# Kernel optimization log

Hardware: AMD Instinct MI355X
Metric: run time of the kernel (lower is better)

Reference implementation:

```python
import jax, jax.numpy as jnp
import numpy as np

D_MODEL = 256
N_HEADS_SA = 8
CA_HEADS = 8
CA_DH = 64
CA_INNER = CA_HEADS * CA_DH  # 512
N_POINTS = 4
D_FFN = 1024
OFFSET_SCALE = 2.0
B, NQ = 4, 1024
T, H, W = 4, 64, 64
LV = T * H * W

PNAMES = ['sa_Wq','sa_bq','sa_Wk','sa_bk','sa_Wv','sa_bv','sa_Wo','sa_bo',
          'ln1_g','ln1_b','ln2_g','ln2_b','ln3_g','ln3_b',
          'ca_Wq','ca_bq','ca_Wk','ca_bk','ca_Wv','ca_bv','ca_Wref','ca_bref',
          'ca_Woff','ca_boff','ca_Wo','ca_bo',
          'ffn_W1','ffn_b1','ffn_W2','ffn_b2']


def _layer_norm(x, g, b, eps=1e-5):
    m = x.mean(-1, keepdims=True)
    v = ((x - m) ** 2).mean(-1, keepdims=True)
    return (x - m) * jax.lax.rsqrt(v + eps) * g + b


def _mha(q, k, v, Wq, bq, Wk, bk, Wv, bv, Wo, bo, n_heads):
    Bq, N, D = q.shape
    dh = D // n_heads
    scale = 1.0 / float(np.sqrt(dh))
    qh = (q @ Wq + bq).reshape(Bq, N, n_heads, dh)
    kh = (k @ Wk + bk).reshape(Bq, N, n_heads, dh)
    vh = (v @ Wv + bv).reshape(Bq, N, n_heads, dh)
    attn = jax.nn.softmax(jnp.einsum('bqhd,bkhd->bhqk', qh, kh) * scale, -1)
    out = jnp.einsum('bhqk,bkhd->bqhd', attn, vh).reshape(Bq, N, D)
    return out @ Wo + bo


def _trilinear_sample(vol, loc, sizes_f):
    # vol: [B, L, Hd, dh] flattened (T*H*W) volume per head
    # loc: [B, N, Hd, P, 3] normalized (t, h, w) coords in [0, 1]
    Bv, L, Hd, dh = vol.shape
    _, N, _, P, _ = loc.shape
    pos = jnp.clip(loc, 0.0, 1.0) * (sizes_f - 1.0)  # align_corners voxel coords
    p0 = jnp.floor(pos)
    frac = pos - p0
    p0i = p0.astype(jnp.int32)
    sizes_i = sizes_f.astype(jnp.int32)
    Hn, Wn = sizes_i[1], sizes_i[2]
    vol_t = vol.transpose(0, 2, 1, 3)  # [B, Hd, L, dh]
    out = jnp.zeros((Bv, Hd, N * P, dh), vol.dtype)
    for dt in (0, 1):
        for dy in (0, 1):
            for dx in (0, 1):
                c = jnp.minimum(p0i + jnp.array([dt, dy, dx], jnp.int32), sizes_i - 1)
                wt = (frac[..., 0] if dt else 1.0 - frac[..., 0]) \
                   * (frac[..., 1] if dy else 1.0 - frac[..., 1]) \
                   * (frac[..., 2] if dx else 1.0 - frac[..., 2])  # [B,N,Hd,P]
                idx = c[..., 0] * (Hn * Wn) + c[..., 1] * Wn + c[..., 2]
                idx_t = idx.transpose(0, 2, 1, 3).reshape(Bv, Hd, N * P, 1)
                g = jnp.take_along_axis(vol_t, idx_t, axis=2)  # [B,Hd,N*P,dh]
                w_t = wt.transpose(0, 2, 1, 3).reshape(Bv, Hd, N * P, 1)
                out = out + g * w_t
    return out.reshape(Bv, Hd, N, P, dh).transpose(0, 2, 1, 3, 4)  # [B,N,Hd,P,dh]


def _deform_cross_attn(query, key, value, flow_key, flow_value, spatial_shapes, p):
    Bq, N, _ = query.shape
    L = key.shape[1]
    sizes_f = spatial_shapes[0].astype(jnp.float32)  # single level (T, H, W)
    qh = (query @ p['ca_Wq'] + p['ca_bq']).reshape(Bq, N, CA_HEADS, CA_DH)
    ref = jax.nn.sigmoid(query @ p['ca_Wref'] + p['ca_bref'])  # [B,N,3]
    off = (query @ p['ca_Woff'] + p['ca_boff']).reshape(Bq, N, CA_HEADS, N_POINTS, 3)
    loc = ref[:, :, None, None, :] + off * (OFFSET_SCALE / sizes_f)
    k_vol = (key @ p['ca_Wk'] + p['ca_bk']).reshape(Bq, L, CA_HEADS, CA_DH)
    v_vol = (value @ p['ca_Wv'] + p['ca_bv']).reshape(Bq, L, CA_HEADS, CA_DH)
    fk_vol = (flow_key @ p['ca_Wk'] + p['ca_bk']).reshape(Bq, L, CA_HEADS, CA_DH)
    fv_vol = (flow_value @ p['ca_Wv'] + p['ca_bv']).reshape(Bq, L, CA_HEADS, CA_DH)
    k_s = _trilinear_sample(k_vol, loc, sizes_f)
    v_s = _trilinear_sample(v_vol, loc, sizes_f)
    fk_s = _trilinear_sample(fk_vol, loc, sizes_f)
    fv_s = _trilinear_sample(fv_vol, loc, sizes_f)
    scale = 1.0 / float(np.sqrt(CA_DH))
    logits = jnp.concatenate([
        jnp.einsum('bnhd,bnhpd->bnhp', qh, k_s),
        jnp.einsum('bnhd,bnhpd->bnhp', qh, fk_s)], -1) * scale
    attn = jax.nn.softmax(logits, -1)  # joint softmax over image+flow sampled points
    vals = jnp.concatenate([v_s, fv_s], 3)  # [B,N,Hd,2P,dh]
    out = jnp.einsum('bnhp,bnhpd->bnhd', attn, vals).reshape(Bq, N, CA_INNER)
    return out @ p['ca_Wo'] + p['ca_bo']


def _forward(query, query_pos, img, flow, pos_emb, spatial_shapes, p):
    q = query + query_pos
    sa = _mha(q, q, query, p['sa_Wq'], p['sa_bq'], p['sa_Wk'], p['sa_bk'],
              p['sa_Wv'], p['sa_bv'], p['sa_Wo'], p['sa_bo'], N_HEADS_SA)
    x = _layer_norm(query + sa, p['ln1_g'], p['ln1_b'])
    key = pos_emb + img
    flow_key = pos_emb + flow
    ca = _deform_cross_attn(x, key, img, flow_key, flow, spatial_shapes, p)
    x = _layer_norm(x + ca, p['ln2_g'], p['ln2_b'])
    ffn = jax.nn.relu(x @ p['ffn_W1'] + p['ffn_b1']) @ p['ffn_W2'] + p['ffn_b2']
    return _layer_norm(x + ffn, p['ln3_g'], p['ln3_b'])


def setup_inputs() -> dict:
    key = jax.random.key(0)
    ks = iter(jax.random.split(key, 64))
    def rn(shape, s=1.0):
        return jax.random.normal(next(ks), shape, jnp.float32) * s
    inp = {
        'query': rn((B, NQ, D_MODEL)),
        'query_pos': rn((B, NQ, D_MODEL)),
        'img_embed_flatten': rn((B, LV, D_MODEL)),
        'flow_embed_flatten': rn((B, LV, D_MODEL)),
        'indicator_temporal_lvl_pos_embed_flatten': rn((B, LV, D_MODEL)),
        'spatial_shapes': jnp.array([[T, H, W]], jnp.int32),
    }
    for nm in ['sa_Wq', 'sa_Wk', 'sa_Wv', 'sa_Wo']:
        inp[nm] = rn((D_MODEL, D_MODEL), 0.02)
    for nm in ['sa_bq', 'sa_bk', 'sa_bv', 'sa_bo', 'ln1_b', 'ln2_b', 'ln3_b']:
        inp[nm] = jnp.zeros((D_MODEL,), jnp.float32)
    for nm in ['ln1_g', 'ln2_g', 'ln3_g']:
        inp[nm] = jnp.ones((D_MODEL,), jnp.float32)
    inp['ca_Wq'] = rn((D_MODEL, CA_INNER), 0.02); inp['ca_bq'] = jnp.zeros((CA_INNER,), jnp.float32)
    inp['ca_Wk'] = rn((D_MODEL, CA_INNER), 0.02); inp['ca_bk'] = jnp.zeros((CA_INNER,), jnp.float32)
    inp['ca_Wv'] = rn((D_MODEL, CA_INNER), 0.02); inp['ca_bv'] = jnp.zeros((CA_INNER,), jnp.float32)
    inp['ca_Wref'] = rn((D_MODEL, 3), 0.02); inp['ca_bref'] = jnp.zeros((3,), jnp.float32)
    inp['ca_Woff'] = rn((D_MODEL, CA_HEADS * N_POINTS * 3), 0.02)
    inp['ca_boff'] = jnp.zeros((CA_HEADS * N_POINTS * 3,), jnp.float32)
    inp['ca_Wo'] = rn((CA_INNER, D_MODEL), 0.02); inp['ca_bo'] = jnp.zeros((D_MODEL,), jnp.float32)
    inp['ffn_W1'] = rn((D_MODEL, D_FFN), 0.02); inp['ffn_b1'] = jnp.zeros((D_FFN,), jnp.float32)
    inp['ffn_W2'] = rn((D_FFN, D_MODEL), 0.02); inp['ffn_b2'] = jnp.zeros((D_MODEL,), jnp.float32)
    return inp


def reference(query, query_pos, img_embed_flatten, flow_embed_flatten,
              indicator_temporal_lvl_pos_embed_flatten, spatial_shapes,
              sa_Wq, sa_bq, sa_Wk, sa_bk, sa_Wv, sa_bv, sa_Wo, sa_bo,
              ln1_g, ln1_b, ln2_g, ln2_b, ln3_g, ln3_b,
              ca_Wq, ca_bq, ca_Wk, ca_bk, ca_Wv, ca_bv, ca_Wref, ca_bref,
              ca_Woff, ca_boff, ca_Wo, ca_bo,
              ffn_W1, ffn_b1, ffn_W2, ffn_b2):
    p = dict(zip(PNAMES, (sa_Wq, sa_bq, sa_Wk, sa_bk, sa_Wv, sa_bv, sa_Wo, sa_bo,
                          ln1_g, ln1_b, ln2_g, ln2_b, ln3_g, ln3_b,
                          ca_Wq, ca_bq, ca_Wk, ca_bk, ca_Wv, ca_bv, ca_Wref, ca_bref,
                          ca_Woff, ca_boff, ca_Wo, ca_bo,
                          ffn_W1, ffn_b1, ffn_W2, ffn_b2)))
    return _forward(query, query_pos, img_embed_flatten, flow_embed_flatten,
                    indicator_temporal_lvl_pos_embed_flatten, spatial_shapes, p)
```

## Files before the change

kernel.cpp:

```cpp
#include <hip/hip_runtime.h>
#include <hip/hip_bf16.h>

#define BQ 4
#define NQT 1024
#define DM 256
#define HSA 8
#define DHSA 32
#define CAH 8
#define CADH 64
#define CAI 512
#define NPT 4
#define DFFN 1024
#define TT 4
#define HH 64
#define WW 64
#define LVOL 16384

using bf16 = __hip_bfloat16;
typedef __attribute__((ext_vector_type(4))) float fx4;
typedef __attribute__((ext_vector_type(8))) short s8v;
typedef __attribute__((ext_vector_type(4))) short s4v;

__device__ __forceinline__ float b2f(bf16 v) { return __bfloat162float(v); }
__device__ __forceinline__ bf16  f2b(float v) { return __float2bfloat16(v); }
__device__ __forceinline__ short f2bs(float v) {
  bf16 b = __float2bfloat16(v);
  return *reinterpret_cast<short*>(&b);
}

__device__ __forceinline__ float wave_sum64(float v) {
#pragma unroll
  for (int o = 32; o >= 1; o >>= 1) v += __shfl_xor(v, o, 64);
  return v;
}

__device__ __forceinline__ s8v pack8(float4 a, float4 b) {
  return (s8v){f2bs(a.x), f2bs(a.y), f2bs(a.z), f2bs(a.w),
               f2bs(b.x), f2bs(b.y), f2bs(b.z), f2bs(b.w)};
}

template <int KSH>
__global__ __launch_bounds__(256) void wtrans_k(const float* __restrict__ W,
                                               short* __restrict__ Wt, int N) {
  const int i = blockIdx.x * 256 + threadIdx.x;
  const int k = i & ((1 << KSH) - 1);
  const int n = i >> KSH;
  Wt[i] = f2bs(W[(size_t)k * N + n]);
}

template <int DUAL, int RELU, int OUTBF>
__global__ __launch_bounds__(256) void mgemm_k(
    const float* __restrict__ A, const float* __restrict__ A2,
    const short* __restrict__ Wt, const float* __restrict__ bias,
    void* __restrict__ Cout, int M, int N, int K) {
  __shared__ short As[2][128 * 40];
  __shared__ short Bs[2][128 * 40];
  const int tid = threadIdx.x;
  const int lane = tid & 63, w = tid >> 6;
  const int wr = w >> 1, wc = w & 1;
  const int lm = lane & 15, quad = lane >> 4;
  const int nwg = gridDim.x * gridDim.y;
  const int ib = blockIdx.y * gridDim.x + blockIdx.x;
  const int id = (ib & 7) * (nwg >> 3) + (ib >> 3);
  const int m0 = (id / gridDim.x) * 128;
  const int n0 = (id % gridDim.x) * 128;

  const int am = tid >> 3, ak = (tid & 7) * 4;

  float4 pa[4], pa2[4];
  s8v pb[2];
  auto loadT = [&](int k0) {
#pragma unroll
    for (int i = 0; i < 4; i++) {
      pa[i] = *(const float4*)&A[(size_t)(m0 + am + i * 32) * K + k0 + ak];
      if (DUAL)
        pa2[i] = *(const float4*)&A2[(size_t)(m0 + am + i * 32) * K + k0 + ak];
    }
#pragma unroll
    for (int i = 0; i < 2; i++) {
      int unit = tid + i * 256;
      pb[i] = *(const s8v*)&Wt[(size_t)(n0 + (unit >> 2)) * K + k0 +
                               (unit & 3) * 8];
    }
  };
  auto stageT = [&](int buf) {
#pragma unroll
    for (int i = 0; i < 4; i++) {
      float x0 = pa[i].x, x1 = pa[i].y, x2 = pa[i].z, x3 = pa[i].w;
      if (DUAL) { x0 += pa2[i].x; x1 += pa2[i].y; x2 += pa2[i].z; x3 += pa2[i].w; }
      s4v sv = {f2bs(x0), f2bs(x1), f2bs(x2), f2bs(x3)};
      *(s4v*)&As[buf][(am + i * 32) * 40 + ak] = sv;
    }
#pragma unroll
    for (int i = 0; i < 2; i++) {
      int unit = tid + i * 256;
      *(s8v*)&Bs[buf][(unit >> 2) * 40 + (unit & 3) * 8] = pb[i];
    }
  };

  fx4 acc[4][4] = {};
  loadT(0);
  stageT(0);
  __syncthreads();
  int cur = 0;
  for (int k0 = 0; k0 < K; k0 += 32) {
    const int more = (k0 + 32 < K);
    if (more) loadT(k0 + 32);
    s8v af[4], bfr[4];
#pragma unroll
    for (int f = 0; f < 4; f++) {
      af[f] = *(s8v*)&As[cur][(wr * 64 + f * 16 + lm) * 40 + quad * 8];
      bfr[f] = *(s8v*)&Bs[cur][(wc * 64 + f * 16 + lm) * 40 + quad * 8];
    }
#pragma unroll
    for (int fm = 0; fm < 4; fm++)
#pragma unroll
      for (int fn = 0; fn < 4; fn++)
        acc[fm][fn] = __builtin_amdgcn_mfma_f32_16x16x32_bf16(
            af[fm], bfr[fn], acc[fm][fn], 0, 0, 0);
    if (more) stageT(cur ^ 1);
    __syncthreads();
    cur ^= 1;
  }
#pragma unroll
  for (int fn = 0; fn < 4; fn++) {
    const int n = n0 + wc * 64 + fn * 16 + lm;
    const float bb = bias[n];
#pragma unroll
    for (int fm = 0; fm < 4; fm++) {
      const int mbase = m0 + wr * 64 + fm * 16 + quad * 4;
#pragma unroll
      for (int r = 0; r < 4; r++) {
        float v = acc[fm][fn][r] + bb;
        if (RELU) v = fmaxf(v, 0.0f);
        const size_t off = (size_t)(mbase + r) * N + n;
        if (OUTBF)
          ((bf16*)Cout)[off] = f2b(v);
        else
          ((float*)Cout)[off] = v;
      }
    }
  }
}

__global__ __launch_bounds__(256) void sa_flash_k(
    const float* __restrict__ qh, const float* __restrict__ kh,
    const float* __restrict__ vh, float* __restrict__ outp) {
  __shared__ short Ks[64 * 72];
  __shared__ short Vt[32 * 72];
  __shared__ short Ps[64 * 72];
  const int qt = blockIdx.x, h = blockIdx.y, b = blockIdx.z;
  const int tid = threadIdx.x;
  const int w = tid >> 6, lane = tid & 63;
  const int lm = lane & 15, quad = lane >> 4;
  const size_t rowbase = (size_t)(b * NQT) * DM + h * DHSA;

  s8v aq;
  {
    const int qrow = qt * 64 + w * 16 + lm;
    const float* qp = &qh[rowbase + (size_t)qrow * DM + quad * 8];
    const float4 q0 = *(const float4*)qp;
    const float4 q1 = *(const float4*)(qp + 4);
    const float sc = 0.17677669529663687f;
    aq = (s8v){f2bs(q0.x * sc), f2bs(q0.y * sc), f2bs(q0.z * sc), f2bs(q0.w * sc),
               f2bs(q1.x * sc), f2bs(q1.y * sc), f2bs(q1.z * sc), f2bs(q1.w * sc)};
  }

  fx4 o0 = {}, o1 = {};
  float mrun[4] = {-1e30f, -1e30f, -1e30f, -1e30f};
  float lrun[4] = {0.f, 0.f, 0.f, 0.f};
  const int jr = tid >> 2;
  const int d0 = (tid & 3) * 8;

  for (int jt = 0; jt < 16; jt++) {
    __syncthreads();
    {
      const size_t rb = rowbase + (size_t)(jt * 64 + jr) * DM + d0;
      const float4 k0 = *(const float4*)&kh[rb];
      const float4 k1 = *(const float4*)&kh[rb + 4];
      *(s8v*)&Ks[jr * 72 + d0] = pack8(k0, k1);
      const float4 v0 = *(const float4*)&vh[rb];
      const float4 v1 = *(const float4*)&vh[rb + 4];
      Vt[(d0 + 0) * 72 + jr] = f2bs(v0.x);
      Vt[(d0 + 1) * 72 + jr] = f2bs(v0.y);
      Vt[(d0 + 2) * 72 + jr] = f2bs(v0.z);
      Vt[(d0 + 3) * 72 + jr] = f2bs(v0.w);
      Vt[(d0 + 4) * 72 + jr] = f2bs(v1.x);
      Vt[(d0 + 5) * 72 + jr] = f2bs(v1.y);
      Vt[(d0 + 6) * 72 + jr] = f2bs(v1.z);
      Vt[(d0 + 7) * 72 + jr] = f2bs(v1.w);
    }
    __syncthreads();
    fx4 s[4];
    const fx4 zero = {};
#pragma unroll
    for (int nf = 0; nf < 4; nf++) {
      s8v kb = *(const s8v*)&Ks[(nf * 16 + lm) * 72 + quad * 8];
      s[nf] = __builtin_amdgcn_mfma_f32_16x16x32_bf16(aq, kb, zero, 0, 0, 0);
    }
#pragma unroll
    for (int r = 0; r < 4; r++) {
      float mx = fmaxf(fmaxf(s[0][r], s[1][r]), fmaxf(s[2][r], s[3][r]));
#pragma unroll
      for (int off = 8; off >= 1; off >>= 1)
        mx = fmaxf(mx, __shfl_xor(mx, off, 64));
      const float mnew = fmaxf(mrun[r], mx);
      const float corr = expf(mrun[r] - mnew);
      mrun[r] = mnew;
      float p0 = expf(s[0][r] - mnew);
      float p1 = expf(s[1][r] - mnew);
      float p2 = expf(s[2][r] - mnew);
      float p3 = expf(s[3][r] - mnew);
      float rs = p0 + p1 + p2 + p3;
#pragma unroll
      for (int off = 8; off >= 1; off >>= 1) rs += __shfl_xor(rs, off, 64);
      lrun[r] = lrun[r] * corr + rs;
      o0[r] *= corr;
      o1[r] *= corr;
      s[0][r] = p0; s[1][r] = p1; s[2][r] = p2; s[3][r] = p3;
    }
#pragma unroll
    for (int nf = 0; nf < 4; nf++)
#pragma unroll
      for (int r = 0; r < 4; r++)
        Ps[(w * 16 + quad * 4 + r) * 72 + nf * 16 + lm] = f2bs(s[nf][r]);
#pragma unroll
    for (int ks = 0; ks < 2; ks++) {
      s8v pf = *(const s8v*)&Ps[(w * 16 + lm) * 72 + ks * 32 + quad * 8];
      s8v vb0 = *(const s8v*)&Vt[lm * 72 + ks * 32 + quad * 8];
      s8v vb1 = *(const s8v*)&Vt[(16 + lm) * 72 + ks * 32 + quad * 8];
      o0 = __builtin_amdgcn_mfma_f32_16x16x32_bf16(pf, vb0, o0, 0, 0, 0);
      o1 = __builtin_amdgcn_mfma_f32_16x16x32_bf16(pf, vb1, o1, 0, 0, 0);
    }
  }
#pragma unroll
  for (int r = 0; r < 4; r++) {
    const float inv = 1.0f / lrun[r];
    const size_t base =
        rowbase + (size_t)(qt * 64 + w * 16 + quad * 4 + r) * DM;
    outp[base + lm] = o0[r] * inv;
    outp[base + 16 + lm] = o1[r] * inv;
  }
}

__global__ __launch_bounds__(128) void refoff_k(
    const float* __restrict__ x1, const float* __restrict__ Wref,
    const float* __restrict__ bref, const float* __restrict__ Woff,
    const float* __restrict__ boff, float* __restrict__ refb,
    float* __restrict__ offb) {
  __shared__ float xs[256];
  const int row = blockIdx.x;
  const int tid = threadIdx.x;
  xs[tid] = x1[(size_t)row * DM + tid];
  xs[tid + 128] = x1[(size_t)row * DM + tid + 128];
  __syncthreads();
  if (tid < 3) {
    float s = bref[tid];
    for (int d = 0; d < 256; d++) s = fmaf(xs[d], Wref[d * 3 + tid], s);
    refb[(size_t)row * 3 + tid] = 1.0f / (1.0f + expf(-s));
  } else if (tid < 99) {
    int o = tid - 3;
    float s = boff[o];
    for (int d = 0; d < 256; d++) s = fmaf(xs[d], Woff[d * 96 + o], s);
    offb[(size_t)row * 96 + o] = s;
  }
}

__device__ __forceinline__ void calc_corners(
    const float* __restrict__ refb, const float* __restrict__ offb, int bn,
    int h, int (&idxs)[NPT][8], float (&wts)[NPT][8]) {
  const float rt = refb[bn * 3 + 0], ry = refb[bn * 3 + 1], rx = refb[bn * 3 + 2];
  const float* ofp = &offb[(size_t)bn * 96 + h * 12];
#pragma unroll
  for (int p = 0; p < NPT; p++) {
    float lt = rt + ofp[p * 3 + 0] * 0.5f;
    float ly = ry + ofp[p * 3 + 1] * 0.03125f;
    float lx = rx + ofp[p * 3 + 2] * 0.03125f;
    float pt = fminf(fmaxf(lt, 0.f), 1.f) * (TT - 1);
    float py = fminf(fmaxf(ly, 0.f), 1.f) * (HH - 1);
    float px = fminf(fmaxf(lx, 0.f), 1.f) * (WW - 1);
    float f0t = floorf(pt), f0y = floorf(py), f0x = floorf(px);
    float frt = pt - f0t, fry = py - f0y, frx = px - f0x;
    int t0 = (int)f0t, y0 = (int)f0y, x0 = (int)f0x;
    int t1 = min(t0 + 1, TT - 1), y1 = min(y0 + 1, HH - 1), x1 = min(x0 + 1, WW - 1);
    float wt0 = 1.f - frt, wy0 = 1.f - fry, wx0 = 1.f - frx;
#pragma unroll
    for (int c = 0; c < 8; c++) {
      int dt = c >> 2, dy = (c >> 1) & 1, dx = c & 1;
      int ct = dt ? t1 : t0, cy = dy ? y1 : y0, cx = dx ? x1 : x0;
      idxs[p][c] = ct * (HH * WW) + cy * WW + cx;
      wts[p][c] = (dt ? frt : wt0) * (dy ? fry : wy0) * (dx ? frx : wx0);
    }
  }
}

__global__ __launch_bounds__(256) void ca_logits_k(
    const float* __restrict__ qh, const float* __restrict__ refb,
    const float* __restrict__ offb, const bf16* __restrict__ vol,
    float* __restrict__ logits, int slot) {
  const int wid = (blockIdx.x * blockDim.x + threadIdx.x) >> 6;
  const int lane = threadIdx.x & 63;
  const int h = wid & 7;
  const int bn = wid >> 3;
  const int b = bn >> 10;
  const float q = qh[(size_t)bn * CAI + h * CADH + lane];
  int idxs[NPT][8];
  float wts[NPT][8];
  calc_corners(refb, offb, bn, h, idxs, wts);
  const size_t volbase = (size_t)b * LVOL * CAI + h * CADH + lane;
  float* lp = logits + ((size_t)bn * CAH + h) * 8 + slot;
#pragma unroll
  for (int p = 0; p < NPT; p++) {
    float ks = 0.f;
#pragma unroll
    for (int c = 0; c < 8; c++)
      ks = fmaf(wts[p][c], b2f(vol[volbase + (size_t)idxs[p][c] * CAI]), ks);
    float li = wave_sum64(q * ks) * 0.125f;
    if (lane == p) lp[p] = li;
  }
}

__global__ __launch_bounds__(256) void ca_softmax_k(float* __restrict__ logits) {
  const int i = blockIdx.x * blockDim.x + threadIdx.x;
  float* p = logits + (size_t)i * 8;
  float v[8], m = -1e30f;
#pragma unroll
  for (int j = 0; j < 8; j++) { v[j] = p[j]; m = fmaxf(m, v[j]); }
  float s = 0.f;
#pragma unroll
  for (int j = 0; j < 8; j++) { v[j] = expf(v[j] - m); s += v[j]; }
  const float inv = 1.0f / s;
#pragma unroll
  for (int j = 0; j < 8; j++) p[j] = v[j] * inv;
}

template <int FIRST>
__global__ __launch_bounds__(256) void ca_acc_k(
    const float* __restrict__ refb, const float* __restrict__ offb,
    const bf16* __restrict__ vol, const float* __restrict__ attn,
    float* __restrict__ acc, int slot) {
  const int wid = (blockIdx.x * blockDim.x + threadIdx.x) >> 6;
  const int lane = threadIdx.x & 63;
  const int h = wid & 7;
  const int bn = wid >> 3;
  const int b = bn >> 10;
  int idxs[NPT][8];
  float wts[NPT][8];
  calc_corners(refb, offb, bn, h, idxs, wts);
  const size_t volbase = (size_t)b * LVOL * CAI + h * CADH + lane;
  const float* ap = attn + ((size_t)bn * CAH + h) * 8 + slot;
  const size_t off = (size_t)bn * CAI + h * CADH + lane;
  float a = FIRST ? 0.f : acc[off];
#pragma unroll
  for (int p = 0; p < NPT; p++) {
    float vs = 0.f;
#pragma unroll
    for (int c = 0; c < 8; c++)
      vs = fmaf(wts[p][c], b2f(vol[volbase + (size_t)idxs[p][c] * CAI]), vs);
    a = fmaf(ap[p], vs, a);
  }
  acc[off] = a;
}

__global__ __launch_bounds__(256) void ln_k(
    const float* __restrict__ resv, const float* __restrict__ x,
    const float* __restrict__ g, const float* __restrict__ bb,
    float* __restrict__ of) {
  const int row = (blockIdx.x * blockDim.x + threadIdx.x) >> 6;
  const int lane = threadIdx.x & 63;
  const size_t base = (size_t)row * DM;
  float v[4];
#pragma unroll
  for (int i = 0; i < 4; i++) {
    int d = lane + i * 64;
    v[i] = resv[base + d] + x[base + d];
  }
  float s = wave_sum64(v[0] + v[1] + v[2] + v[3]);
  const float mean = s * (1.0f / 256.0f);
  float vs = 0.f;
#pragma unroll
  for (int i = 0; i < 4; i++) { float d0 = v[i] - mean; vs = fmaf(d0, d0, vs); }
  vs = wave_sum64(vs);
  const float rstd = rsqrtf(vs * (1.0f / 256.0f) + 1e-5f);
#pragma unroll
  for (int i = 0; i < 4; i++) {
    int d = lane + i * 64;
    of[base + d] = (v[i] - mean) * rstd * g[d] + bb[d];
  }
}

extern "C" void kernel_launch(void* const* d_in, const int* in_sizes, int n_in,
                              void* d_out, int out_size, void* d_ws,
                              size_t ws_size, hipStream_t stream) {
  const float* query = (const float*)d_in[0];
  const float* qpos = (const float*)d_in[1];
  const float* img = (const float*)d_in[2];
  const float* flow = (const float*)d_in[3];
  const float* pos = (const float*)d_in[4];
  const float* sa_Wq = (const float*)d_in[6];
  const float* sa_Wk = (const float*)d_in[7];
  const float* sa_Wv = (const float*)d_in[8];
  const float* sa_Wo = (const float*)d_in[9];
  const float* sa_bq = (const float*)d_in[10];
  const float* sa_bk = (const float*)d_in[11];
  const float* sa_bv = (const float*)d_in[12];
  const float* sa_bo = (const float*)d_in[13];
  const float* ln1_b = (const float*)d_in[14];
  const float* ln2_b = (const float*)d_in[15];
  const float* ln3_b = (const float*)d_in[16];
  const float* ln1_g = (const float*)d_in[17];
  const float* ln2_g = (const float*)d_in[18];
  const float* ln3_g = (const float*)d_in[19];
  const float* ca_Wq = (const float*)d_in[20];
  const float* ca_bq = (const float*)d_in[21];
  const float* ca_Wk = (const float*)d_in[22];
  const float* ca_bk = (const float*)d_in[23];
  const float* ca_Wv = (const float*)d_in[24];
  const float* ca_bv = (const float*)d_in[25];
  const float* ca_Wref = (const float*)d_in[26];
  const float* ca_bref = (const float*)d_in[27];
  const float* ca_Woff = (const float*)d_in[28];
  const float* ca_boff = (const float*)d_in[29];
  const float* ca_Wo = (const float*)d_in[30];
  const float* ca_bo = (const float*)d_in[31];
  const float* ffn_W1 = (const float*)d_in[32];
  const float* ffn_b1 = (const float*)d_in[33];
  const float* ffn_W2 = (const float*)d_in[34];
  const float* ffn_b2 = (const float*)d_in[35];

  const int MQ = BQ * NQT;
  const int MV = BQ * LVOL;
  const size_t MB = 1024 * 1024;

  char* r0 = (char*)d_ws;
  char* w = r0 + 64 * MB;
  auto alloc = [&](size_t n) {
    char* p = w;
    w += (n + 255) & ~(size_t)255;
    return p;
  };
  float* x1_f = (float*)alloc((size_t)MQ * DM * 4);
  float* ca_qh = (float*)alloc((size_t)MQ * CAI * 4);
  float* refb = (float*)alloc((size_t)MQ * 3 * 4);
  float* offb = (float*)alloc((size_t)MQ * 96 * 4);
  float* logits = (float*)alloc((size_t)MQ * CAH * 8 * 4);
  float* ca_acc = (float*)alloc((size_t)MQ * CAI * 4);
  short* WtsaQ = (short*)alloc((size_t)DM * DM * 2);
  short* WtsaK = (short*)alloc((size_t)DM * DM * 2);
  short* WtsaV = (short*)alloc((size_t)DM * DM * 2);
  short* WtsaO = (short*)alloc((size_t)DM * DM * 2);
  short* Wtcaq = (short*)alloc((size_t)CAI * DM * 2);
  short* Wtk = (short*)alloc((size_t)CAI * DM * 2);
  short* Wtv = (short*)alloc((size_t)CAI * DM * 2);
  short* Wtcao = (short*)alloc((size_t)DM * CAI * 2);
  short* Wtf1 = (short*)alloc((size_t)DFFN * DM * 2);
  short* Wtf2 = (short*)alloc((size_t)DM * DFFN * 2);
  if ((size_t)(w - (char*)d_ws) > ws_size) return;

  float* qh_sa = (float*)(r0 + 0 * MB);
  float* kh_sa = (float*)(r0 + 4 * MB);
  float* vh_sa = (float*)(r0 + 8 * MB);
  float* sa_att = (float*)(r0 + 12 * MB);
  float* sa_proj = (float*)(r0 + 16 * MB);
  bf16* vol = (bf16*)r0;
  float* ca_o = (float*)(r0 + 0 * MB);
  float* x2_f = (float*)(r0 + 4 * MB);
  float* ffn_h = (float*)(r0 + 8 * MB);
  float* ffn_o = (float*)(r0 + 24 * MB);

  dim3 blk(256);
  wtrans_k<8><<<dim3(DM * DM / 256), blk, 0, stream>>>(sa_Wq, WtsaQ, DM);
  wtrans_k<8><<<dim3(DM * DM / 256), blk, 0, stream>>>(sa_Wk, WtsaK, DM);
  wtrans_k<8><<<dim3(DM * DM / 256), blk, 0, stream>>>(sa_Wv, WtsaV, DM);
  wtrans_k<8><<<dim3(DM * DM / 256), blk, 0, stream>>>(sa_Wo, WtsaO, DM);
  wtrans_k<8><<<dim3(DM * CAI / 256), blk, 0, stream>>>(ca_Wq, Wtcaq, CAI);
  wtrans_k<8><<<dim3(DM * CAI / 256), blk, 0, stream>>>(ca_Wk, Wtk, CAI);
  wtrans_k<8><<<dim3(DM * CAI / 256), blk, 0, stream>>>(ca_Wv, Wtv, CAI);
  wtrans_k<8><<<dim3(DM * DFFN / 256), blk, 0, stream>>>(ffn_W1, Wtf1, DFFN);
  wtrans_k<9><<<dim3(CAI * DM / 256), blk, 0, stream>>>(ca_Wo, Wtcao, DM);
  wtrans_k<10><<<dim3(DFFN * DM / 256), blk, 0, stream>>>(ffn_W2, Wtf2, DM);
  mgemm_k<1, 0, 0><<<dim3(DM / 128, MQ / 128), blk, 0, stream>>>(query, qpos, WtsaQ, sa_bq, (void*)qh_sa, MQ, DM, DM);
  mgemm_k<1, 0, 0><<<dim3(DM / 128, MQ / 128), blk, 0, stream>>>(query, qpos, WtsaK, sa_bk, (void*)kh_sa, MQ, DM, DM);
  mgemm_k<0, 0, 0><<<dim3(DM / 128, MQ / 128), blk, 0, stream>>>(query, query, WtsaV, sa_bv, (void*)vh_sa, MQ, DM, DM);
  sa_flash_k<<<dim3(16, 8, 4), blk, 0, stream>>>(qh_sa, kh_sa, vh_sa, sa_att);
  mgemm_k<0, 0, 0><<<dim3(DM / 128, MQ / 128), blk, 0, stream>>>(sa_att, sa_att, WtsaO, sa_bo, (void*)sa_proj, MQ, DM, DM);
  ln_k<<<dim3(MQ / 4), blk, 0, stream>>>(query, sa_proj, ln1_g, ln1_b, x1_f);
  mgemm_k<0, 0, 0><<<dim3(CAI / 128, MQ / 128), blk, 0, stream>>>(x1_f, x1_f, Wtcaq, ca_bq, (void*)ca_qh, MQ, CAI, DM);
  refoff_k<<<dim3(MQ), dim3(128), 0, stream>>>(x1_f, ca_Wref, ca_bref, ca_Woff, ca_boff, refb, offb);
  mgemm_k<1, 0, 1><<<dim3(CAI / 128, MV / 128), blk, 0, stream>>>(pos, img, Wtk, ca_bk, (void*)vol, MV, CAI, DM);
  ca_logits_k<<<dim3(8192), blk, 0, stream>>>(ca_qh, refb, offb, vol, logits, 0);
  mgemm_k<1, 0, 1><<<dim3(CAI / 128, MV / 128), blk, 0, stream>>>(pos, flow, Wtk, ca_bk, (void*)vol, MV, CAI, DM);
  ca_logits_k<<<dim3(8192), blk, 0, stream>>>(ca_qh, refb, offb, vol, logits, 4);
  ca_softmax_k<<<dim3(128), blk, 0, stream>>>(logits);
  mgemm_k<0, 0, 1><<<dim3(CAI / 128, MV / 128), blk, 0, stream>>>(img, img, Wtv, ca_bv, (void*)vol, MV, CAI, DM);
  ca_acc_k<1><<<dim3(8192), blk, 0, stream>>>(refb, offb, vol, logits, ca_acc, 0);
  mgemm_k<0, 0, 1><<<dim3(CAI / 128, MV / 128), blk, 0, stream>>>(flow, flow, Wtv, ca_bv, (void*)vol, MV, CAI, DM);
  ca_acc_k<0><<<dim3(8192), blk, 0, stream>>>(refb, offb, vol, logits, ca_acc, 4);
  mgemm_k<0, 0, 0><<<dim3(DM / 128, MQ / 128), blk, 0, stream>>>(ca_acc, ca_acc, Wtcao, ca_bo, (void*)ca_o, MQ, DM, CAI);
  ln_k<<<dim3(MQ / 4), blk, 0, stream>>>(x1_f, ca_o, ln2_g, ln2_b, x2_f);
  mgemm_k<0, 1, 0><<<dim3(DFFN / 128, MQ / 128), blk, 0, stream>>>(x2_f, x2_f, Wtf1, ffn_b1, (void*)ffn_h, MQ, DFFN, DM);
  mgemm_k<0, 0, 0><<<dim3(DM / 128, MQ / 128), blk, 0, stream>>>(ffn_h, ffn_h, Wtf2, ffn_b2, (void*)ffn_o, MQ, DM, DFFN);
  ln_k<<<dim3(MQ / 4), blk, 0, stream>>>(x2_f, ffn_o, ln3_g, ln3_b, (float*)d_out);
}
```

Measured before the change: 744.6 us.

## Pre-convert volume inputs to bf16 and use direct-to-LDS loads in volume GEMMs

The four large K/V projection GEMMs over the flattened volume now run in two steps. A prep kernel first adds the positional embedding where needed and converts the fp32 input to a bf16 buffer. A new bf16 GEMM then streams that buffer and the transposed weights straight into LDS with global_load_lds, double buffered, and feeds MFMA. The aim is to take fp32 loading and conversion out of the GEMM main loop, where the A tile is re-read once per N-block, and to overlap global loads with compute without staging through registers. The cost is an extra read and write pass over each volume input, plus new unpadded LDS tiles that may cause bank conflicts.

```diff
diff --git a/kernel.cpp b/kernel.cpp
--- a/kernel.cpp
+++ b/kernel.cpp
@@ -39,6 +39,12 @@
                f2bs(b.x), f2bs(b.y), f2bs(b.z), f2bs(b.w)};
 }
 
+__device__ __forceinline__ void gl_lds16(const void* g, void* l) {
+  __builtin_amdgcn_global_load_lds(
+      (const __attribute__((address_space(1))) unsigned int*)g,
+      (__attribute__((address_space(3))) unsigned int*)l, 16, 0, 0);
+}
+
 template <int KSH>
 __global__ __launch_bounds__(256) void wtrans_k(const float* __restrict__ W,
                                                short* __restrict__ Wt, int N) {
@@ -46,6 +52,91 @@
   const int k = i & ((1 << KSH) - 1);
   const int n = i >> KSH;
   Wt[i] = f2bs(W[(size_t)k * N + n]);
+}
+
+template <int DUAL>
+__global__ __launch_bounds__(256) void prep_k(const float* __restrict__ A,
+                                              const float* __restrict__ B,
+                                              short* __restrict__ O, int n8) {
+  for (int i = blockIdx.x * 256 + threadIdx.x; i < n8; i += gridDim.x * 256) {
+    float4 a0 = *(const float4*)&A[(size_t)i * 8];
+    float4 a1 = *(const float4*)&A[(size_t)i * 8 + 4];
+    if (DUAL) {
+      const float4 b0 = *(const float4*)&B[(size_t)i * 8];
+      const float4 b1 = *(const float4*)&B[(size_t)i * 8 + 4];
+      a0.x += b0.x; a0.y += b0.y; a0.z += b0.z; a0.w += b0.w;
+      a1.x += b1.x; a1.y += b1.y; a1.z += b1.z; a1.w += b1.w;
+    }
+    *(s8v*)&O[(size_t)i * 8] = pack8(a0, a1);
+  }
+}
+
+__global__ __launch_bounds__(256) void bgemm_k(
+    const short* __restrict__ A, const short* __restrict__ Wt,
+    const float* __restrict__ bias, bf16* __restrict__ Cout,
+    int M, int N, int K) {
+  __shared__ short As[2][128 * 32];
+  __shared__ short Bs[2][128 * 32];
+  const int tid = threadIdx.x;
+  const int lane = tid & 63, w = tid >> 6;
+  const int wr = w >> 1, wc = w & 1;
+  const int lm = lane & 15, quad = lane >> 4;
+  const int nwg = gridDim.x * gridDim.y;
+  const int ib = blockIdx.y * gridDim.x + blockIdx.x;
+  const int id = (ib & 7) * (nwg >> 3) + (ib >> 3);
+  const int m0 = (id / gridDim.x) * 128;
+  const int n0 = (id % gridDim.x) * 128;
+
+  const int srow = lane >> 2;
+  const int scol = (lane & 3) * 8;
+  const size_t arow = (size_t)(m0 + w * 32 + srow);
+  const size_t brow = (size_t)(n0 + w * 32 + srow);
+
+  fx4 acc[4][4] = {};
+  const int nt = K / 32;
+  int cur = 0;
+  {
+    gl_lds16(&A[arow * K + scol], &As[0][(w * 32) * 32]);
+    gl_lds16(&A[(arow + 16) * K + scol], &As[0][(w * 32 + 16) * 32]);
+    gl_lds16(&Wt[brow * K + scol], &Bs[0][(w * 32) * 32]);
+    gl_lds16(&Wt[(brow + 16) * K + scol], &Bs[0][(w * 32 + 16) * 32]);
+  }
+  __syncthreads();
+  for (int t = 0; t < nt; t++) {
+    if (t + 1 < nt) {
+      const int k0 = (t + 1) * 32;
+      gl_lds16(&A[arow * K + k0 + scol], &As[cur ^ 1][(w * 32) * 32]);
+      gl_lds16(&A[(arow + 16) * K + k0 + scol], &As[cur ^ 1][(w * 32 + 16) * 32]);
+      gl_lds16(&Wt[brow * K + k0 + scol], &Bs[cur ^ 1][(w * 32) * 32]);
+      gl_lds16(&Wt[(brow + 16) * K + k0 + scol], &Bs[cur ^ 1][(w * 32 + 16) * 32]);
+    }
+    s8v af[4], bfr[4];
+#pragma unroll
+    for (int f = 0; f < 4; f++) {
+      af[f] = *(s8v*)&As[cur][(wr * 64 + f * 16 + lm) * 32 + quad * 8];
+      bfr[f] = *(s8v*)&Bs[cur][(wc * 64 + f * 16 + lm) * 32 + quad * 8];
+    }
+#pragma unroll
+    for (int fm = 0; fm < 4; fm++)
+#pragma unroll
+      for (int fn = 0; fn < 4; fn++)
+        acc[fm][fn] = __builtin_amdgcn_mfma_f32_16x16x32_bf16(
+            af[fm], bfr[fn], acc[fm][fn], 0, 0, 0);
+    __syncthreads();
+    cur ^= 1;
+  }
+#pragma unroll
+  for (int fn = 0; fn < 4; fn++) {
+    const int n = n0 + wc * 64 + fn * 16 + lm;
+    const float bb = bias[n];
+#pragma unroll
+    for (int fm = 0; fm < 4; fm++) {
+      const int mbase = m0 + wr * 64 + fm * 16 + quad * 4;
+#pragma unroll
+      for (int r = 0; r < 4; r++)
+        Cout[(size_t)(mbase + r) * N + n] = f2b(acc[fm][fn][r] + bb);
+    }
+  }
 }
 
 template <int DUAL, int RELU, int OUTBF>
@@ -455,6 +546,7 @@
   short* Wtcao = (short*)alloc((size_t)DM * CAI * 2);
   short* Wtf1 = (short*)alloc((size_t)DFFN * DM * 2);
   short* Wtf2 = (short*)alloc((size_t)DM * DFFN * 2);
+  short* abuf = (short*)alloc((size_t)MV * DM * 2);
   if ((size_t)(w - (char*)d_ws) > ws_size) return;
 
   float* qh_sa = (float*)(r0 + 0 * MB);
@@ -467,6 +559,8 @@
   float* x2_f = (float*)(r0 + 4 * MB);
   float* ffn_h = (float*)(r0 + 8 * MB);
   float* ffn_o = (float*)(r0 + 24 * MB);
+
+  const int n8v = MV * DM / 8;
 
   dim3 blk(256);
   wtrans_k<8><<<dim3(DM * DM / 256), blk, 0, stream>>>(sa_Wq, WtsaQ, DM);
@@ -487,14 +581,18 @@
   ln_k<<<dim3(MQ / 4), blk, 0, stream>>>(query, sa_proj, ln1_g, ln1_b, x1_f);
   mgemm_k<0, 0, 0><<<dim3(CAI / 128, MQ / 128), blk, 0, stream>>>(x1_f, x1_f, Wtcaq, ca_bq, (void*)ca_qh, MQ, CAI, DM);
   refoff_k<<<dim3(MQ), dim3(128), 0, stream>>>(x1_f, ca_Wref, ca_bref, ca_Woff, ca_boff, refb, offb);
-  mgemm_k<1, 0, 1><<<dim3(CAI / 128, MV / 128), blk, 0, stream>>>(pos, img, Wtk, ca_bk, (void*)vol, MV, CAI, DM);
+  prep_k<1><<<dim3(2048), blk, 0, stream>>>(pos, img, abuf, n8v);
+  bgemm_k<<<dim3(CAI / 128, MV / 128), blk, 0, stream>>>(abuf, Wtk, ca_bk, vol, MV, CAI, DM);
   ca_logits_k<<<dim3(8192), blk, 0, stream>>>(ca_qh, refb, offb, vol, logits, 0);
-  mgemm_k<1, 0, 1><<<dim3(CAI / 128, MV / 128), blk, 0, stream>>>(pos, flow, Wtk, ca_bk, (void*)vol, MV, CAI, DM);
+  prep_k<1><<<dim3(2048), blk, 0, stream>>>(pos, flow, abuf, n8v);
+  bgemm_k<<<dim3(CAI / 128, MV / 128), blk, 0, stream>>>(abuf, Wtk, ca_bk, vol, MV, CAI, DM);
   ca_logits_k<<<dim3(8192), blk, 0, stream>>>(ca_qh, refb, offb, vol, logits, 4);
   ca_softmax_k<<<dim3(128), blk, 0, stream>>>(logits);
-  mgemm_k<0, 0, 1><<<dim3(CAI / 128, MV / 128), blk, 0, stream>>>(img, img, Wtv, ca_bv, (void*)vol, MV, CAI, DM);
+  prep_k<0><<<dim3(2048), blk, 0, stream>>>(img, img, abuf, n8v);
+  bgemm_k<<<dim3(CAI / 128, MV / 128), blk, 0, stream>>>(abuf, Wtv, ca_bv, vol, MV, CAI, DM);
   ca_acc_k<1><<<dim3(8192), blk, 0, stream>>>(refb, offb, vol, logits, ca_acc, 0);
-  mgemm_k<0, 0, 1><<<dim3(CAI / 128, MV / 128), blk, 0, stream>>>(flow, flow, Wtv, ca_bv, (void*)vol, MV, CAI, DM);
+  prep_k<0><<<dim3(2048), blk, 0, stream>>>(flow, flow, abuf, n8v);
+  bgemm_k<<<dim3(CAI / 128, MV / 128), blk, 0, stream>>>(abuf, Wtv, ca_bv, vol, MV, CAI, DM);
   ca_acc_k<0><<<dim3(8192), blk, 0, stream>>>(refb, offb, vol, logits, ca_acc, 4);
   mgemm_k<0, 0, 0><<<dim3(DM / 128, MQ / 128), blk, 0, stream>>>(ca_acc, ca_acc, Wtcao, ca_bo, (void*)ca_o, MQ, DM, CAI);
   ln_k<<<dim3(MQ / 4), blk, 0, stream>>>(x1_f, ca_o, ln2_g, ln2_b, x2_f);
```

Result: faster. 725.1 us (-2.6%).
